# Kernel optimization log

Measured on AMD Instinct MI355X. Metric: run time of the kernel, lower is better.

## Reference

```python
import jax, jax.numpy as jnp
import numpy as np

B, N, P, K, C = 8, 4096, 4096, 32, 128  # batch, points, npoint, neighbors, channels (=mlp[-1])
W_OUT = 16  # weightnet output channels (from Linear(16*mlp[-1], mlp[-1]))
EPS = 1e-5


def setup_inputs() -> dict:
    key = jax.random.key(0)
    ks = jax.random.split(key, 9)
    xyz = jax.random.normal(ks[0], (B, P, 3), jnp.float32)
    points = jax.random.normal(ks[1], (B, N, C), jnp.float32)
    local_coordinates = jax.random.normal(ks[2], (B, P, K, 3), jnp.float32)
    neighbor_lists = jax.random.randint(ks[3], (B, P, K), 0, N)
    data_idx = jax.random.randint(ks[4], (B,), 0, B)
    Ww = jax.random.normal(ks[5], (3, W_OUT), jnp.float32) * 0.1   # weightnet (pointwise linear 3->16)
    bw = jnp.zeros((W_OUT,), jnp.float32)
    Wl = jax.random.normal(ks[6], (W_OUT * C, C), jnp.float32) * 0.02  # nn.Linear(16*mlp[-1], mlp[-1])
    bl = jnp.zeros((C,), jnp.float32)
    gamma = jnp.ones((C,), jnp.float32)   # BatchNorm1d weight
    beta = jnp.zeros((C,), jnp.float32)   # BatchNorm1d bias
    return {"xyz": xyz, "points": points, "local_coordinates": local_coordinates,
            "neighbor_lists": neighbor_lists, "data_idx": data_idx,
            "Ww": Ww, "bw": bw, "Wl": Wl, "bl": bl, "gamma": gamma, "beta": beta}


def reference(xyz, points, local_coordinates, neighbor_lists, data_idx, Ww, bw, Wl, bl, gamma, beta):
    b, p, k, _ = local_coordinates.shape
    c = points.shape[-1]
    # weightnet: pointwise map of 3-D local coordinates to 16 weight channels -> [B,P,K,16]
    weights = local_coordinates @ Ww + bw
    # irregular neighbor gather: data[b,p,k,:] = points[b, neighbor_lists[b,p,k], :] -> [B,P,K,C]
    data = points[jnp.arange(b)[:, None, None], neighbor_lists]
    # per-point weighted aggregation over K neighbors: [B,P,C,16] -> flatten to [B,P,C*16]
    new_points = jnp.einsum('bpkc,bpkw->bpcw', data, weights).reshape(b, p, c * weights.shape[-1])
    # batch reindex via data_idx
    new_points = new_points[data_idx]
    # linear tail: [B,P,C]
    new_points = new_points @ Wl + bl
    # BatchNorm1d over channel dim (training-mode batch stats), then ReLU: [B,C,P]
    x = new_points.transpose(0, 2, 1)
    mean = x.mean(axis=(0, 2), keepdims=True)
    var = x.var(axis=(0, 2), keepdims=True)
    x = (x - mean) * jax.lax.rsqrt(var + EPS) * gamma[None, :, None] + beta[None, :, None]
    return xyz, jax.nn.relu(x)
```

## Files before the change

### kernel.cpp

```cpp
#include <hip/hip_runtime.h>

#define Bn 8
#define Nn 4096
#define Pn 4096
#define Kn 32
#define Cn 128

using float4v = __attribute__((ext_vector_type(4))) float;
using short8  = __attribute__((ext_vector_type(8))) short;

__device__ __forceinline__ unsigned short bf16b(float f) {
  union { float f; unsigned u; } v; v.f = f;
  unsigned r = v.u + 0x7FFFu + ((v.u >> 16) & 1u);
  return (unsigned short)(r >> 16);
}

__device__ __forceinline__ unsigned pkhi(float x, float y) {
  return __builtin_amdgcn_perm(__float_as_uint(y), __float_as_uint(x), 0x07060302u);
}

__global__ __launch_bounds__(256) void prep(const float* __restrict__ Wl,
                                            unsigned short* __restrict__ WlT,
                                            const float* __restrict__ xyz,
                                            float* __restrict__ out,
                                            float* __restrict__ gacc) {
  __shared__ unsigned short tile[128 * 33];
  const int t = threadIdx.x, blk = blockIdx.x;
  if (blk < 64) {
#pragma unroll
    for (int i = 0; i < 16; ++i) {
      int idx = i * 256 + t;
      int kl = idx >> 7, n = idx & 127;
      tile[n * 33 + kl] = bf16b(Wl[(size_t)(blk * 32 + kl) * 128 + n]);
    }
    __syncthreads();
#pragma unroll
    for (int i = 0; i < 16; ++i) {
      int idx = i * 256 + t;
      int n = idx >> 5, kl = idx & 31;
      WlT[(size_t)n * 2048 + blk * 32 + kl] = tile[n * 33 + kl];
    }
  } else {
    if (blk == 64) gacc[t] = 0.f;
    const int i0 = (blk - 64) * 3072 + t * 12;
#pragma unroll
    for (int i = 0; i < 3; ++i)
      *(float4v*)(out + i0 + i * 4) = *(const float4v*)(xyz + i0 + i * 4);
  }
}

__global__ __launch_bounds__(512, 8) void fused(
    const float* __restrict__ points, const float* __restrict__ lc,
    const int* __restrict__ nl, const int* __restrict__ didx,
    const float* __restrict__ Ww, const float* __restrict__ bwv,
    const unsigned short* __restrict__ WlT, const float* __restrict__ blv,
    float* __restrict__ xout, float* __restrict__ gacc) {
  __shared__ unsigned short Mlds[32 * 256];
  __shared__ int nlds[32 * 32];
  __shared__ float red[256];

  const int t = threadIdx.x, lane = t & 63, w = t >> 6;
  const int l15 = lane & 15, q = lane >> 4;
  const int b = blockIdx.x & 7;
  const int pg = blockIdx.x >> 3;
  const int p0 = pg * 32;
  const int db = didx[b];
  const char* __restrict__ pbase = (const char*)(points + (size_t)db * Nn * Cn);

  {
    int2 nv = *(const int2*)(nl + (size_t)(db * Pn + p0) * Kn + t * 2);
    nv.x <<= 9; nv.y <<= 9;
    *(int2*)&nlds[t * 2] = nv;
  }

  const float Ww0 = Ww[l15], Ww1 = Ww[16 + l15], Ww2 = Ww[32 + l15];
  const float bw0 = bwv[l15];

  short8 af[4];
#pragma unroll
  for (int i = 0; i < 4; ++i) {
    const int p = p0 + w * 4 + i;
    const int pk = (db * Pn + p) * Kn;
    const float* __restrict__ lcp = lc + (size_t)(pk + q * 8) * 3;
    float la[24];
#pragma unroll
    for (int v = 0; v < 6; ++v) *(float4v*)&la[v * 4] = *(const float4v*)(lcp + v * 4);
#pragma unroll
    for (int j = 0; j < 8; ++j) {
      float ww = bw0 + la[3 * j] * Ww0 + la[3 * j + 1] * Ww1 + la[3 * j + 2] * Ww2;
      af[i][j] = (short)bf16b(ww);
    }
  }

  float4v acc[2];
  acc[0] = (float4v){0.f, 0.f, 0.f, 0.f};
  acc[1] = (float4v){0.f, 0.f, 0.f, 0.f};

  __syncthreads();

  const unsigned short* __restrict__ bp =
      WlT + (size_t)(w * 16 + l15) * 2048 + q * 8;
  const unsigned cvoff = (unsigned)(l15 * 4);

#define ISSUE(i, ct, fdst)                                                 \
  {                                                                        \
    const int pi_ = w * 4 + (i);                                           \
    int nk_[8];                                                            \
    *(int4*)&nk_[0] = *(const int4*)&nlds[pi_ * 32 + q * 8];               \
    *(int4*)&nk_[4] = *(const int4*)&nlds[pi_ * 32 + q * 8 + 4];           \
    _Pragma("unroll") for (int j = 0; j < 8; ++j)                          \
        fdst[j] = *(const float*)(pbase + ((unsigned)nk_[j] + cvoff +      \
                                           (unsigned)((ct) * 64)));        \
  }

#define FIN(i, fsrc)                                                       \
  {                                                                        \
    const int pi_ = w * 4 + (i);                                           \
    union { short8 s; unsigned u[4]; } bv_;                                \
    bv_.u[0] = pkhi(fsrc[0], fsrc[1]);                                     \
    bv_.u[1] = pkhi(fsrc[2], fsrc[3]);                                     \
    bv_.u[2] = pkhi(fsrc[4], fsrc[5]);                                     \
    bv_.u[3] = pkhi(fsrc[6], fsrc[7]);                                     \
    float4v d_ = {0.f, 0.f, 0.f, 0.f};                                     \
    d_ = __builtin_amdgcn_mfma_f32_16x16x32_bf16(af[i], bv_.s, d_, 0, 0, 0); \
    const unsigned off_ = (unsigned)(pi_ * 512 +                           \
        ((l15 * 32 + q * 8) ^ ((pi_ & 7) << 4)));                          \
    uint2 u_;                                                              \
    u_.x = pkhi(d_[0], d_[1]);                                             \
    u_.y = pkhi(d_[2], d_[3]);                                             \
    *(uint2*)((char*)Mlds + off_) = u_;                                    \
  }

  float fb0[8], fb1[8];

  for (int ct = 0; ct < 8; ++ct) {
    ISSUE(0, ct, fb0)
    ISSUE(1, ct, fb1)
    FIN(0, fb0)
    ISSUE(2, ct, fb0)
    FIN(1, fb1)
    ISSUE(3, ct, fb1)
    FIN(2, fb0)
    FIN(3, fb1)
    __syncthreads();
#pragma unroll
    for (int ks = 0; ks < 8; ++ks) {
      const unsigned ax = (unsigned)((ks * 64 + q * 16) ^ ((l15 & 7) << 4));
      short8 a0 = *(const short8*)((const char*)Mlds + l15 * 512 + ax);
      short8 a1 = *(const short8*)((const char*)Mlds + (16 + l15) * 512 + ax);
      short8 b0 = *(const short8*)(bp + ct * 256 + ks * 32);
      acc[0] = __builtin_amdgcn_mfma_f32_16x16x32_bf16(a0, b0, acc[0], 0, 0, 0);
      acc[1] = __builtin_amdgcn_mfma_f32_16x16x32_bf16(a1, b0, acc[1], 0, 0, 0);
    }
    __syncthreads();
  }
#undef ISSUE
#undef FIN

  {
    const int ch = w * 16 + l15;
    const float bb = blv[ch];
    float s = 0.f, sq = 0.f;
#pragma unroll
    for (int rt = 0; rt < 2; ++rt) {
      float4v o;
#pragma unroll
      for (int r = 0; r < 4; ++r) {
        float v = acc[rt][r] + bb; o[r] = v; s += v; sq += v * v;
      }
      *(float4v*)(xout + ((size_t)(b * Cn + ch)) * Pn + p0 + rt * 16 + q * 4) = o;
    }
    s += __shfl_xor(s, 16); s += __shfl_xor(s, 32);
    sq += __shfl_xor(sq, 16); sq += __shfl_xor(sq, 32);
    if (lane < 16) { red[ch] = s; red[128 + ch] = sq; }
  }
  __syncthreads();
  if (t < 256) atomicAdd(&gacc[t], red[t]);
}

__global__ __launch_bounds__(256) void finalize_ln(float* __restrict__ x,
                                                   const float* __restrict__ gacc,
                                                   const float* __restrict__ gamma,
                                                   const float* __restrict__ beta) {
  const int idx = blockIdx.x * 256 + threadIdx.x;
  const int fi = idx * 4;
  const int c = (fi >> 12) & 127;
  const float inv = 1.f / 32768.f;
  const float mean = gacc[c] * inv;
  const float var = gacc[128 + c] * inv - mean * mean;
  const float scale = rsqrtf(var + 1e-5f) * gamma[c];
  const float shift = beta[c] - mean * scale;
  float4v v = *(float4v*)(x + fi);
#pragma unroll
  for (int r = 0; r < 4; ++r) v[r] = fmaxf(v[r] * scale + shift, 0.f);
  *(float4v*)(x + fi) = v;
}

extern "C" void kernel_launch(void* const* d_in, const int* in_sizes, int n_in,
                              void* d_out, int out_size, void* d_ws, size_t ws_size,
                              hipStream_t stream) {
  const float* xyz    = (const float*)d_in[0];
  const float* points = (const float*)d_in[1];
  const float* lc     = (const float*)d_in[2];
  const int*   nl     = (const int*)d_in[3];
  const int*   didx   = (const int*)d_in[4];
  const float* Ww     = (const float*)d_in[5];
  const float* bw     = (const float*)d_in[6];
  const float* Wl     = (const float*)d_in[7];
  const float* bl     = (const float*)d_in[8];
  const float* gamma  = (const float*)d_in[9];
  const float* beta   = (const float*)d_in[10];

  float* out  = (float*)d_out;
  float* xout = out + (size_t)Bn * Pn * 3;
  unsigned short* WlT = (unsigned short*)d_ws;
  float* gacc = (float*)((char*)d_ws + (size_t)512 * 1024);

  prep<<<96, 256, 0, stream>>>(Wl, WlT, xyz, out, gacc);
  fused<<<1024, 512, 0, stream>>>(points, lc, nl, didx, Ww, bw, WlT, bl,
                                  xout, gacc);
  finalize_ln<<<4096, 256, 0, stream>>>(xout, gacc, gamma, beta);
}
```

Baseline: 203.5 us.

## Halve block tile and double-buffer LDS to overlap gather with GEMM

The block size drops from 512 to 256 threads with 16 points per block, and the grid doubles to 2048 blocks. Each wave now computes 32 output channels, so it reuses one A fragment for two B fragments. The per-point weighted aggregation tile is double-buffered in LDS: the neighbor gather and the first MFMA for the next channel tile are issued before the GEMM on the current tile and finished after it, with s_setprio raised around the GEMM. This is meant to hide gather latency behind matrix work, at the cost of more blocks, more gacc atomics, and twice the reads of the weight matrix across the grid.

```diff
diff --git a/kernel.cpp b/kernel.cpp
--- a/kernel.cpp
+++ b/kernel.cpp
@@ -49,21 +49,21 @@
   }
 }
 
-__global__ __launch_bounds__(512, 8) void fused(
+__global__ __launch_bounds__(256, 4) void fused(
     const float* __restrict__ points, const float* __restrict__ lc,
     const int* __restrict__ nl, const int* __restrict__ didx,
     const float* __restrict__ Ww, const float* __restrict__ bwv,
     const unsigned short* __restrict__ WlT, const float* __restrict__ blv,
     float* __restrict__ xout, float* __restrict__ gacc) {
-  __shared__ unsigned short Mlds[32 * 256];
-  __shared__ int nlds[32 * 32];
+  __shared__ unsigned short Mlds[2][16 * 256];
+  __shared__ int nlds[16 * 32];
   __shared__ float red[256];
 
   const int t = threadIdx.x, lane = t & 63, w = t >> 6;
   const int l15 = lane & 15, q = lane >> 4;
   const int b = blockIdx.x & 7;
   const int pg = blockIdx.x >> 3;
-  const int p0 = pg * 32;
+  const int p0 = pg * 16;
   const int db = didx[b];
   const char* __restrict__ pbase = (const char*)(points + (size_t)db * Nn * Cn);
 
@@ -99,7 +99,7 @@
   __syncthreads();
 
   const unsigned short* __restrict__ bp =
-      WlT + (size_t)(w * 16 + l15) * 2048 + q * 8;
+      WlT + (size_t)(w * 32 + l15) * 2048 + q * 8;
   const unsigned cvoff = (unsigned)(l15 * 4);
 
 #define ISSUE(i, ct, fdst)                                                 \
@@ -113,7 +113,7 @@
                                            (unsigned)((ct) * 64)));        \
   }
 
-#define FIN(i, fsrc)                                                       \
+#define FIN(i, bsel, fsrc)                                                 \
   {                                                                        \
     const int pi_ = w * 4 + (i);                                           \
     union { short8 s; unsigned u[4]; } bv_;                                \
@@ -123,7 +123,7 @@
     bv_.u[3] = pkhi(fsrc[6], fsrc[7]);                                     \
     float4v d_ = {0.f, 0.f, 0.f, 0.f};                                     \
     d_ = __builtin_amdgcn_mfma_f32_16x16x32_bf16(af[i], bv_.s, d_, 0, 0, 0); \
-    const unsigned off_ = (unsigned)(pi_ * 512 +                           \
+    const unsigned off_ = (unsigned)((bsel) * 8192 + pi_ * 512 +           \
         ((l15 * 32 + q * 8) ^ ((pi_ & 7) << 4)));                          \
     uint2 u_;                                                              \
     u_.x = pkhi(d_[0], d_[1]);                                             \
@@ -131,51 +131,63 @@
     *(uint2*)((char*)Mlds + off_) = u_;                                    \
   }
 
-  float fb0[8], fb1[8];
-
+  float r0[8], r1[8];
+
+  ISSUE(0, 0, r0)
+  ISSUE(1, 0, r1)
+  FIN(0, 0, r0) ISSUE(2, 0, r0)
+  FIN(1, 0, r1) ISSUE(3, 0, r1)
+  FIN(2, 0, r0)
+  FIN(3, 0, r1)
+  __syncthreads();
+
+#pragma unroll
   for (int ct = 0; ct < 8; ++ct) {
-    ISSUE(0, ct, fb0)
-    ISSUE(1, ct, fb1)
-    FIN(0, fb0)
-    ISSUE(2, ct, fb0)
-    FIN(1, fb1)
-    ISSUE(3, ct, fb1)
-    FIN(2, fb0)
-    FIN(3, fb1)
-    __syncthreads();
+    const int cur = ct & 1, nxt = cur ^ 1;
+    if (ct < 7) {
+      ISSUE(0, ct + 1, r0)
+      ISSUE(1, ct + 1, r1)
+    }
+    const char* mb = (const char*)Mlds + cur * 8192;
+    __builtin_amdgcn_s_setprio(1);
 #pragma unroll
     for (int ks = 0; ks < 8; ++ks) {
       const unsigned ax = (unsigned)((ks * 64 + q * 16) ^ ((l15 & 7) << 4));
-      short8 a0 = *(const short8*)((const char*)Mlds + l15 * 512 + ax);
-      short8 a1 = *(const short8*)((const char*)Mlds + (16 + l15) * 512 + ax);
+      short8 a  = *(const short8*)(mb + l15 * 512 + ax);
       short8 b0 = *(const short8*)(bp + ct * 256 + ks * 32);
-      acc[0] = __builtin_amdgcn_mfma_f32_16x16x32_bf16(a0, b0, acc[0], 0, 0, 0);
-      acc[1] = __builtin_amdgcn_mfma_f32_16x16x32_bf16(a1, b0, acc[1], 0, 0, 0);
+      short8 b1 = *(const short8*)(bp + 32768 + ct * 256 + ks * 32);
+      acc[0] = __builtin_amdgcn_mfma_f32_16x16x32_bf16(a, b0, acc[0], 0, 0, 0);
+      acc[1] = __builtin_amdgcn_mfma_f32_16x16x32_bf16(a, b1, acc[1], 0, 0, 0);
+    }
+    __builtin_amdgcn_s_setprio(0);
+    if (ct < 7) {
+      FIN(0, nxt, r0) ISSUE(2, ct + 1, r0)
+      FIN(1, nxt, r1) ISSUE(3, ct + 1, r1)
+      FIN(2, nxt, r0)
+      FIN(3, nxt, r1)
     }
     __syncthreads();
   }
 #undef ISSUE
 #undef FIN
 
-  {
-    const int ch = w * 16 + l15;
+#pragma unroll
+  for (int nt = 0; nt < 2; ++nt) {
+    const int ch = w * 32 + nt * 16 + l15;
     const float bb = blv[ch];
     float s = 0.f, sq = 0.f;
-#pragma unroll
-    for (int rt = 0; rt < 2; ++rt) {
-      float4v o;
-#pragma unroll
-      for (int r = 0; r < 4; ++r) {
-        float v = acc[rt][r] + bb; o[r] = v; s += v; sq += v * v;
-      }
-      *(float4v*)(xout + ((size_t)(b * Cn + ch)) * Pn + p0 + rt * 16 + q * 4) = o;
-    }
+    float4v o;
+#pragma unroll
+    for (int r = 0; r < 4; ++r) {
+      float v = acc[nt][r] + bb; o[r] = v; s += v; sq += v * v;
+    }
+    *(float4v*)(xout + ((size_t)(b * Cn + ch)) * Pn + p0 + q * 4) = o;
     s += __shfl_xor(s, 16); s += __shfl_xor(s, 32);
     sq += __shfl_xor(sq, 16); sq += __shfl_xor(sq, 32);
     if (lane < 16) { red[ch] = s; red[128 + ch] = sq; }
   }
   __syncthreads();
-  if (t < 256) atomicAdd(&gacc[t], red[t]);
+  atomicAdd(&gacc[t], red[t]);
 }
 
 __global__ __launch_bounds__(256) void finalize_ln(float* __restrict__ x,
@@ -217,7 +229,7 @@
   float* gacc = (float*)((char*)d_ws + (size_t)512 * 1024);
 
   prep<<<96, 256, 0, stream>>>(Wl, WlT, xyz, out, gacc);
-  fused<<<1024, 512, 0, stream>>>(points, lc, nl, didx, Ww, bw, WlT, bl,
+  fused<<<2048, 256, 0, stream>>>(points, lc, nl, didx, Ww, bw, WlT, bl,
                                   xout, gacc);
   finalize_ln<<<4096, 256, 0, stream>>>(xout, gacc, gamma, beta);
 }
```

New measurement: 240.9 us. 1.18x slower.
